# Optimization experiments

Hardware: AMD Instinct MI355X
Metric: run time of the kernel (lower is better)

The kernel has to match this reference:

```python
import jax, jax.numpy as jnp
import numpy as np

TOPK = 13
ALPHA = 1.0
BETA = 6.0
EPS = 1e-9


def _make_boxes(key, shape, img=640.0, min_sz=10.0, max_sz=110.0):
    k1, k2 = jax.random.split(key)
    cxcy = jax.random.uniform(k1, shape[:-1] + (2,)) * img
    wh = min_sz + jax.random.uniform(k2, shape[:-1] + (2,)) * (max_sz - min_sz)
    return jnp.concatenate([cxcy - wh / 2, cxcy + wh / 2], axis=-1)


def setup_inputs() -> dict:
    key = jax.random.key(0)
    ks = jax.random.split(key, 8)
    B, L, C, n, K = 16, 8400, 1, 32, 68
    pred_scores = jax.random.uniform(ks[0], (B, L, C))
    pred_bboxes = _make_boxes(ks[1], (B, L, 4))
    anchor_points = jax.random.uniform(ks[2], (L, 2)) * 640.0
    gt_labels = jax.random.randint(ks[3], (B, n, 1), 0, C).astype(jnp.int64)
    gt_bboxes = _make_boxes(ks[4], (B, n, 4))
    gt_poses = jax.random.normal(ks[5], (B, n, K, 3))
    gt_vertices = jax.random.normal(ks[6], (B, n, K, 3))
    gt_rotations = jax.random.normal(ks[7], (B, n, 3, 3))
    pad_gt_mask = jnp.ones((B, n, 1), jnp.float32)
    return {"pred_scores": pred_scores, "pred_bboxes": pred_bboxes,
            "anchor_points": anchor_points, "gt_labels": gt_labels,
            "gt_bboxes": gt_bboxes, "gt_poses": gt_poses,
            "gt_vertices": gt_vertices, "gt_rotations": gt_rotations,
            "pad_gt_mask": pad_gt_mask, "bg_index": 1}


def batch_iou_similarity(box1, box2):
    # box1 [B,n,4], box2 [B,L,4] -> [B,n,L]
    b1 = box1[:, :, None, :]
    b2 = box2[:, None, :, :]
    x1y1 = jnp.maximum(b1[..., :2], b2[..., :2])
    x2y2 = jnp.minimum(b1[..., 2:], b2[..., 2:])
    overlap = jnp.clip(x2y2 - x1y1, 0).prod(-1)
    area1 = jnp.clip(b1[..., 2:] - b1[..., :2], 0).prod(-1)
    area2 = jnp.clip(b2[..., 2:] - b2[..., :2], 0).prod(-1)
    return overlap / (area1 + area2 - overlap + EPS)


def check_points_inside_bboxes(points, bboxes):
    # points [L,2], bboxes [B,n,4] -> [B,n,L] float
    x = points[None, None, :, 0]
    y = points[None, None, :, 1]
    xmin, ymin, xmax, ymax = jnp.split(bboxes[:, :, None, :], 4, axis=-1)
    deltas = jnp.stack([x - xmin[..., 0], y - ymin[..., 0],
                        xmax[..., 0] - x, ymax[..., 0] - y], axis=-1)
    return (deltas.min(-1) > EPS).astype(bboxes.dtype)


def gather_topk_anchors(metrics, topk, topk_mask):
    # metrics [B,n,L], topk_mask [B,n,1] -> [B,n,L]
    L = metrics.shape[-1]
    _, topk_idxs = jax.lax.top_k(metrics, topk)  # [B,n,topk]
    is_in_topk = jax.nn.one_hot(topk_idxs, L, dtype=metrics.dtype).sum(-2)
    return is_in_topk * topk_mask


def compute_max_iou_anchor(ious):
    # [B,n,L] -> one-hot over gt dim of per-anchor argmax iou
    n = ious.shape[1]
    idx = ious.argmax(axis=1)  # [B,L]
    return jnp.transpose(jax.nn.one_hot(idx, n, dtype=ious.dtype), (0, 2, 1))


def reference(pred_scores, pred_bboxes, anchor_points, gt_labels, gt_bboxes,
              gt_poses, gt_vertices, gt_rotations, pad_gt_mask, bg_index):
    B, L, C = pred_scores.shape
    n = gt_bboxes.shape[1]
    K = gt_poses.shape[2]

    ious = batch_iou_similarity(gt_bboxes, pred_bboxes)  # [B,n,L]
    ps_t = jnp.transpose(pred_scores, (0, 2, 1))  # [B,C,L]
    lbl = gt_labels[..., 0]  # [B,n]
    bbox_cls_scores = jnp.take_along_axis(ps_t, lbl[:, :, None], axis=1)  # [B,n,L]

    alignment_metrics = (bbox_cls_scores ** ALPHA) * (ious ** BETA)
    is_in_gts = check_points_inside_bboxes(anchor_points, gt_bboxes)
    is_in_topk = gather_topk_anchors(alignment_metrics * is_in_gts, TOPK, pad_gt_mask)
    mask_positive = is_in_topk * is_in_gts * pad_gt_mask  # [B,n,L]
    mask_positive_sum = mask_positive.sum(axis=1)  # [B,L]

    # resolve anchors assigned to multiple gts by max IoU (no-op when none)
    mask_multiple = jnp.broadcast_to((mask_positive_sum[:, None, :] > 1), mask_positive.shape)
    is_max_iou = compute_max_iou_anchor(ious)
    mask_positive = jnp.where(mask_multiple, is_max_iou, mask_positive)
    mask_positive_sum = mask_positive.sum(axis=1)

    batch_ind = jnp.arange(B, dtype=jnp.int32)[:, None]
    assigned_gt_index = mask_positive.argmax(axis=1)  # [B,L]
    assigned_gt_index = assigned_gt_index + batch_ind * n
    flat_idx = assigned_gt_index.reshape(-1)

    assigned_labels = gt_labels.reshape(-1)[flat_idx].reshape(B, L)
    assigned_labels = jnp.where(mask_positive_sum > 0, assigned_labels, bg_index)

    assigned_bboxes = gt_bboxes.reshape(-1, 4)[flat_idx].reshape(B, L, 4)
    assigned_poses = gt_poses.reshape(-1, K, 3)[flat_idx].reshape(B, L, K, 3)
    assigned_vertices = gt_vertices.reshape(-1, K, 3)[flat_idx].reshape(B, L, K, 3)
    assigned_rotations = gt_rotations.reshape(-1, 3, 3)[flat_idx].reshape(B, L, 3, 3)

    scores_oh = jax.nn.one_hot(assigned_labels, C + 1, dtype=pred_scores.dtype)
    keep = jnp.array([i for i in range(C + 1) if i != bg_index], dtype=jnp.int32)
    assigned_scores = scores_oh[..., keep]  # [B,L,C]

    am = alignment_metrics * mask_positive
    max_metrics_per_instance = am.max(axis=-1, keepdims=True)
    max_ious_per_instance = (ious * mask_positive).max(axis=-1, keepdims=True)
    am = am / (max_metrics_per_instance + EPS) * max_ious_per_instance
    am = am.max(axis=1)[:, :, None]  # [B,L,1]
    assigned_scores = assigned_scores * am

    return (assigned_labels, assigned_bboxes, assigned_scores, assigned_poses,
            assigned_vertices, assigned_rotations, assigned_gt_index)
```

## Files before the change

### kernel.cpp

```cpp
#include <hip/hip_runtime.h>

#define Bn 16
#define Ln 8400
#define Cn 1
#define Ngt 32
#define Kpt 68
#define TOPKN 13
#define EPSF 1e-9f
#define CAP 2048

typedef unsigned int u32;
typedef float f4v __attribute__((ext_vector_type(4)));

#define OFF_LABELS   0
#define OFF_BBOXES   134400
#define OFF_SCORES   672000
#define OFF_POSES    806400
#define OFF_VERTS    28224000
#define OFF_ROT      55641600
#define OFF_GTIDX    56851200

__device__ __forceinline__ float iou_box(float gx0, float gy0, float gx1, float gy1,
                                         float4 p) {
    float ix0 = fmaxf(gx0, p.x), iy0 = fmaxf(gy0, p.y);
    float ix1 = fminf(gx1, p.z), iy1 = fminf(gy1, p.w);
    float ov = fmaxf(ix1 - ix0, 0.f) * fmaxf(iy1 - iy0, 0.f);
    float a1 = fmaxf(gx1 - gx0, 0.f) * fmaxf(gy1 - gy0, 0.f);
    float a2 = fmaxf(p.z - p.x, 0.f) * fmaxf(p.w - p.y, 0.f);
    return ov / (a1 + a2 - ov + EPSF);
}

__global__ void __launch_bounds__(256) k1_topk(
    const float* __restrict__ pred_scores, const float* __restrict__ pred_bboxes,
    const float* __restrict__ anchors, const int* __restrict__ gt_labels,
    const float* __restrict__ gt_bboxes, const float* __restrict__ pad_mask,
    u32* __restrict__ posmask)
{
    __shared__ float cmet[CAP];
    __shared__ int   cidx[CAP];
    __shared__ int   count;
    __shared__ float rv[4];
    __shared__ int   rl[4], rc[4];
    __shared__ int   sel[TOPKN];

    const int bi = blockIdx.x;
    const int b = bi >> 5, i = bi & 31;
    const int tid = threadIdx.x;

    if (pad_mask[bi] == 0.f) return;

    const float gx0 = gt_bboxes[bi*4+0];
    const float gy0 = gt_bboxes[bi*4+1];
    const float gx1 = gt_bboxes[bi*4+2];
    const float gy1 = gt_bboxes[bi*4+3];
    const int   label = gt_labels[bi];

    const float4* pb = (const float4*)(pred_bboxes + (size_t)b * Ln * 4);
    const float*  ps = pred_scores + (size_t)b * Ln * Cn;
    const float2* ap = (const float2*)anchors;

    if (tid == 0) count = 0;
    __syncthreads();

    for (int l = tid; l < Ln; l += 256) {
        float2 av = ap[l];
        float dmin = fminf(fminf(av.x - gx0, av.y - gy0),
                           fminf(gx1 - av.x, gy1 - av.y));
        if (dmin > EPSF) {
            float4 pv = pb[l];
            float iou = iou_box(gx0, gy0, gx1, gy1, pv);
            float sc = ps[l * Cn + label];
            float i2 = iou * iou;
            float m = sc * (i2 * i2 * i2);
            if (m > 0.f) {
                int c = atomicAdd(&count, 1);
                if (c < CAP) { cmet[c] = m; cidx[c] = l; }
            }
        }
    }
    __syncthreads();
    int p = min(count, CAP);

    if (p > TOPKN) {
        for (int t = 0; t < TOPKN; t++) {
            float bv = -1.f; int bl = 1 << 30, bc = 0;
            for (int c = tid; c < p; c += 256) {
                float v = cmet[c];
                int l = cidx[c];
                if (v > bv || (v == bv && l < bl)) { bv = v; bl = l; bc = c; }
            }
            #pragma unroll
            for (int off = 32; off > 0; off >>= 1) {
                float ov = __shfl_down(bv, off);
                int ol = __shfl_down(bl, off);
                int oc = __shfl_down(bc, off);
                if (ov > bv || (ov == bv && ol < bl)) { bv = ov; bl = ol; bc = oc; }
            }
            int w = tid >> 6;
            if ((tid & 63) == 0) { rv[w] = bv; rl[w] = bl; rc[w] = bc; }
            __syncthreads();
            if (tid == 0) {
                float fv = rv[0]; int fl = rl[0], fc = rc[0];
                #pragma unroll
                for (int w2 = 1; w2 < 4; w2++) {
                    if (rv[w2] > fv || (rv[w2] == fv && rl[w2] < fl)) {
                        fv = rv[w2]; fl = rl[w2]; fc = rc[w2];
                    }
                }
                sel[t] = fl;
                cmet[fc] = -1.f;
            }
            __syncthreads();
        }
        if (tid < TOPKN) atomicOr(&posmask[(size_t)b * Ln + sel[tid]], 1u << i);
    } else {
        if (tid < p) atomicOr(&posmask[(size_t)b * Ln + cidx[tid]], 1u << i);
        if (tid == 0) {
            int need = TOPKN - p;
            for (int l = 0; need > 0 && l < Ln; l++) {
                bool isc = false;
                for (int j = 0; j < p; j++) isc |= (cidx[j] == l);
                if (isc) continue;
                need--;
                float2 av = ap[l];
                float dmin = fminf(fminf(av.x - gx0, av.y - gy0),
                                   fminf(gx1 - av.x, gy1 - av.y));
                if (dmin > EPSF) atomicOr(&posmask[(size_t)b * Ln + l], 1u << i);
            }
        }
    }
}

__global__ void __launch_bounds__(256) k2_resolve(
    const float* __restrict__ pred_scores, const float* __restrict__ pred_bboxes,
    const int* __restrict__ gt_labels, const float* __restrict__ gt_bboxes,
    const u32* __restrict__ posmask, u32* __restrict__ finalmask,
    int* __restrict__ srcidx, float* __restrict__ met_sel,
    float* __restrict__ maxm, float* __restrict__ maxiou)
{
    int bl = blockIdx.x * 256 + threadIdx.x;
    if (bl >= Bn * Ln) return;
    int b = bl / Ln;
    u32 pm = posmask[bl];
    u32 fm = pm;
    float4 pbox = ((const float4*)pred_bboxes)[bl];
    const float4* gb = (const float4*)(gt_bboxes + (size_t)b * Ngt * 4);
    if (__popc(pm) > 1) {
        float best = -1.f; int bi2 = 0;
        for (int i = 0; i < Ngt; i++) {
            float4 g = gb[i];
            float v = iou_box(g.x, g.y, g.z, g.w, pbox);
            if (v > best) { best = v; bi2 = i; }
        }
        fm = 1u << bi2;
    }
    finalmask[bl] = fm;
    int idx = fm ? (__ffs((int)fm) - 1) : 0;
    int src = b * Ngt + idx;
    srcidx[bl] = src;
    float met = 0.f;
    if (fm) {
        float4 g = gb[idx];
        float iou = iou_box(g.x, g.y, g.z, g.w, pbox);
        float sc = pred_scores[(size_t)bl * Cn + gt_labels[src]];
        float i2 = iou * iou;
        met = sc * (i2 * i2 * i2);
        atomicMax((int*)&maxm[src],   __float_as_int(met));
        atomicMax((int*)&maxiou[src], __float_as_int(iou));
    }
    met_sel[bl] = met;
}

__global__ void __launch_bounds__(256) k3_out(
    const float* __restrict__ gt_poses, const float* __restrict__ gt_verts,
    const u32* __restrict__ finalmask, const int* __restrict__ srcidx,
    const float* __restrict__ met_sel, const float* __restrict__ maxm_a,
    const float* __restrict__ maxiou_a, const int* __restrict__ gt_labels,
    const float* __restrict__ gt_bboxes, const float* __restrict__ gt_rot,
    const int* __restrict__ bg_index_p, float* __restrict__ out)
{
    const int QPER = (Kpt * 3) / 4;
    const int total = Bn * Ln * QPER;
    const int nq = 2 * total;
    const int nrot = Bn * Ln * 9;
    int t = blockIdx.x * 256 + threadIdx.x;
    if (t < nq) {
        const float* ga = gt_poses;
        f4v* outp = (f4v*)(out + OFF_POSES);
        int qq = t;
        if (qq >= total) { qq -= total; ga = gt_verts; outp = (f4v*)(out + OFF_VERTS); }
        int bl = qq / QPER;
        int r = qq - bl * QPER;
        int src = srcidx[bl];
        f4v v = ((const f4v*)ga)[src * QPER + r];
        __builtin_nontemporal_store(v, &outp[qq]);
        return;
    }
    t -= nq;
    if (t < nrot) {
        int bl = t / 9;
        int j = t - bl * 9;
        int src = srcidx[bl];
        __builtin_nontemporal_store(gt_rot[src * 9 + j], &out[OFF_ROT + t]);
        return;
    }
    int bl = t - nrot;
    if (bl >= Bn * Ln) return;
    const int bg = *bg_index_p;
    u32 fm = finalmask[bl];
    int src = srcidx[bl];
    int label = fm ? gt_labels[src] : bg;
    float am = 0.f;
    if (fm) am = met_sel[bl] / (maxm_a[src] + EPSF) * maxiou_a[src];
    int keep0 = (bg == 0) ? 1 : 0;
    float sc = (label == keep0) ? am : 0.f;

    __builtin_nontemporal_store((float)label, &out[OFF_LABELS + bl]);
    __builtin_nontemporal_store(sc,           &out[OFF_SCORES + bl]);
    __builtin_nontemporal_store((float)src,   &out[OFF_GTIDX  + bl]);
    f4v bb = ((const f4v*)gt_bboxes)[src];
    __builtin_nontemporal_store(bb, &((f4v*)(out + OFF_BBOXES))[bl]);
}

extern "C" void kernel_launch(void* const* d_in, const int* in_sizes, int n_in,
                              void* d_out, int out_size, void* d_ws, size_t ws_size,
                              hipStream_t stream)
{
    const float* pred_scores = (const float*)d_in[0];
    const float* pred_bboxes = (const float*)d_in[1];
    const float* anchors     = (const float*)d_in[2];
    const int*   gt_labels   = (const int*)d_in[3];
    const float* gt_bboxes   = (const float*)d_in[4];
    const float* gt_poses    = (const float*)d_in[5];
    const float* gt_verts    = (const float*)d_in[6];
    const float* gt_rot      = (const float*)d_in[7];
    const float* pad_mask    = (const float*)d_in[8];
    const int*   bg_index    = (const int*)d_in[9];

    const int nBL = Bn * Ln;
    u32*   posmask  = (u32*)d_ws;
    float* maxm     = (float*)(posmask + nBL);
    float* maxiou   = maxm + Bn * Ngt;
    u32*   finalmask= (u32*)(maxiou + Bn * Ngt);
    int*   srcidx   = (int*)(finalmask + nBL);
    float* met_sel  = (float*)(srcidx + nBL);

    (void)hipMemsetAsync(posmask, 0, ((size_t)nBL + 2 * Bn * Ngt) * sizeof(u32), stream);

    k1_topk<<<Bn * Ngt, 256, 0, stream>>>(pred_scores, pred_bboxes, anchors,
                                          gt_labels, gt_bboxes, pad_mask, posmask);
    k2_resolve<<<(nBL + 255) / 256, 256, 0, stream>>>(pred_scores, pred_bboxes,
                                                      gt_labels, gt_bboxes, posmask,
                                                      finalmask, srcidx, met_sel,
                                                      maxm, maxiou);
    const int nq = 2 * Bn * Ln * ((Kpt * 3) / 4);
    const int nrot = Bn * Ln * 9;
    const int ntot = nq + nrot + nBL;
    k3_out<<<(ntot + 255) / 256, 256, 0, stream>>>(gt_poses, gt_verts, finalmask,
                                                   srcidx, met_sel, maxm, maxiou,
                                                   gt_labels, gt_bboxes, gt_rot,
                                                   bg_index, (float*)d_out);
}
```

Measured before the change: 308.5 us.

## Replace posmask atomics and memset with per-GT top-k index lists, fuse pose/vertex copies

k1 now writes each GT's 13 selected anchor indices to a compact list instead of atomically OR-ing bits into a B×L mask. It also zeroes the max buffers itself, which removes the memset of the full mask. k2 rebuilds the positive mask per anchor by scanning the shared-memory index lists for its batch. k3 makes each thread copy both the pose and the vertex float4 for one slot, halving the thread count for that section. The cost is 416 comparisons per anchor in k2. Zeroing maxm inside k1 depends on kernel ordering before k2's atomicMax, which holds on a single stream.

```diff
diff --git a/kernel.cpp b/kernel.cpp
--- a/kernel.cpp
+++ b/kernel.cpp
@@ -34,7 +34,7 @@
     const float* __restrict__ pred_scores, const float* __restrict__ pred_bboxes,
     const float* __restrict__ anchors, const int* __restrict__ gt_labels,
     const float* __restrict__ gt_bboxes, const float* __restrict__ pad_mask,
-    u32* __restrict__ posmask)
+    int* __restrict__ selg, float* __restrict__ maxm )
 {
     __shared__ float cmet[CAP];
     __shared__ int   cidx[CAP];
@@ -44,10 +44,15 @@
     __shared__ int   sel[TOPKN];
 
     const int bi = blockIdx.x;
-    const int b = bi >> 5, i = bi & 31;
+    const int b = bi >> 5;
     const int tid = threadIdx.x;
 
-    if (pad_mask[bi] == 0.f) return;
+    { int z = bi * 256 + tid; if (z < 2 * Bn * Ngt) maxm[z] = 0.f; }
+
+    if (pad_mask[bi] == 0.f) {
+        if (tid < TOPKN) selg[bi * TOPKN + tid] = -1;
+        return;
+    }
 
     const float gx0 = gt_bboxes[bi*4+0];
     const float gy0 = gt_bboxes[bi*4+1];
@@ -112,20 +117,20 @@
             }
             __syncthreads();
         }
-        if (tid < TOPKN) atomicOr(&posmask[(size_t)b * Ln + sel[tid]], 1u << i);
+        if (tid < TOPKN) selg[bi * TOPKN + tid] = sel[tid];
     } else {
-        if (tid < p) atomicOr(&posmask[(size_t)b * Ln + cidx[tid]], 1u << i);
+        if (tid < p) selg[bi * TOPKN + tid] = cidx[tid];
         if (tid == 0) {
-            int need = TOPKN - p;
-            for (int l = 0; need > 0 && l < Ln; l++) {
+            int pos = p;
+            for (int l = 0; pos < TOPKN && l < Ln; l++) {
                 bool isc = false;
                 for (int j = 0; j < p; j++) isc |= (cidx[j] == l);
                 if (isc) continue;
-                need--;
                 float2 av = ap[l];
                 float dmin = fminf(fminf(av.x - gx0, av.y - gy0),
                                    fminf(gx1 - av.x, gy1 - av.y));
-                if (dmin > EPSF) atomicOr(&posmask[(size_t)b * Ln + l], 1u << i);
+                selg[bi * TOPKN + pos] = (dmin > EPSF) ? l : -1;
+                pos++;
             }
         }
     }
@@ -134,14 +139,28 @@
 __global__ void __launch_bounds__(256) k2_resolve(
     const float* __restrict__ pred_scores, const float* __restrict__ pred_bboxes,
     const int* __restrict__ gt_labels, const float* __restrict__ gt_bboxes,
-    const u32* __restrict__ posmask, u32* __restrict__ finalmask,
+    const int* __restrict__ selg, u32* __restrict__ finalmask,
     int* __restrict__ srcidx, float* __restrict__ met_sel,
     float* __restrict__ maxm, float* __restrict__ maxiou)
 {
-    int bl = blockIdx.x * 256 + threadIdx.x;
-    if (bl >= Bn * Ln) return;
-    int b = bl / Ln;
-    u32 pm = posmask[bl];
+    __shared__ int ssel[Ngt * TOPKN];
+    const int b = blockIdx.y;
+    const int l = blockIdx.x * 256 + threadIdx.x;
+    for (int z = threadIdx.x; z < Ngt * TOPKN; z += 256)
+        ssel[z] = selg[b * Ngt * TOPKN + z];
+    __syncthreads();
+    if (l >= Ln) return;
+    const int bl = b * Ln + l;
+
+    u32 pm = 0;
+    #pragma unroll 4
+    for (int i = 0; i < Ngt; i++) {
+        u32 hit = 0;
+        #pragma unroll
+        for (int j = 0; j < TOPKN; j++) hit |= (u32)(ssel[i * TOPKN + j] == l);
+        pm |= hit << i;
+    }
+
     u32 fm = pm;
     float4 pbox = ((const float4*)pred_bboxes)[bl];
     const float4* gb = (const float4*)(gt_bboxes + (size_t)b * Ngt * 4);
@@ -180,23 +199,20 @@
     const int* __restrict__ bg_index_p, float* __restrict__ out)
 {
     const int QPER = (Kpt * 3) / 4;
-    const int total = Bn * Ln * QPER;
-    const int nq = 2 * total;
+    const int totalA = Bn * Ln * QPER;
     const int nrot = Bn * Ln * 9;
     int t = blockIdx.x * 256 + threadIdx.x;
-    if (t < nq) {
-        const float* ga = gt_poses;
-        f4v* outp = (f4v*)(out + OFF_POSES);
-        int qq = t;
-        if (qq >= total) { qq -= total; ga = gt_verts; outp = (f4v*)(out + OFF_VERTS); }
-        int bl = qq / QPER;
-        int r = qq - bl * QPER;
+    if (t < totalA) {
+        int bl = t / QPER;
+        int r = t - bl * QPER;
         int src = srcidx[bl];
-        f4v v = ((const f4v*)ga)[src * QPER + r];
-        __builtin_nontemporal_store(v, &outp[qq]);
+        f4v pv = ((const f4v*)gt_poses)[src * QPER + r];
+        f4v vv = ((const f4v*)gt_verts)[src * QPER + r];
+        __builtin_nontemporal_store(pv, &((f4v*)(out + OFF_POSES))[t]);
+        __builtin_nontemporal_store(vv, &((f4v*)(out + OFF_VERTS))[t]);
         return;
     }
-    t -= nq;
+    t -= totalA;
     if (t < nrot) {
         int bl = t / 9;
         int j = t - bl * 9;
@@ -238,24 +254,23 @@
     const int*   bg_index    = (const int*)d_in[9];
 
     const int nBL = Bn * Ln;
-    u32*   posmask  = (u32*)d_ws;
-    float* maxm     = (float*)(posmask + nBL);
+    int*   selg     = (int*)d_ws;
+    float* maxm     = (float*)(selg + Bn * Ngt * TOPKN);
     float* maxiou   = maxm + Bn * Ngt;
     u32*   finalmask= (u32*)(maxiou + Bn * Ngt);
     int*   srcidx   = (int*)(finalmask + nBL);
     float* met_sel  = (float*)(srcidx + nBL);
 
-    (void)hipMemsetAsync(posmask, 0, ((size_t)nBL + 2 * Bn * Ngt) * sizeof(u32), stream);
 
     k1_topk<<<Bn * Ngt, 256, 0, stream>>>(pred_scores, pred_bboxes, anchors,
-                                          gt_labels, gt_bboxes, pad_mask, posmask);
-    k2_resolve<<<(nBL + 255) / 256, 256, 0, stream>>>(pred_scores, pred_bboxes,
-                                                      gt_labels, gt_bboxes, posmask,
-                                                      finalmask, srcidx, met_sel,
-                                                      maxm, maxiou);
-    const int nq = 2 * Bn * Ln * ((Kpt * 3) / 4);
+                                          gt_labels, gt_bboxes, pad_mask,
+                                          selg, maxm);
+    k2_resolve<<<dim3((Ln + 255) / 256, Bn), 256, 0, stream>>>(
+        pred_scores, pred_bboxes, gt_labels, gt_bboxes, selg,
+        finalmask, srcidx, met_sel, maxm, maxiou);
+    const int totalA = Bn * Ln * ((Kpt * 3) / 4);
     const int nrot = Bn * Ln * 9;
-    const int ntot = nq + nrot + nBL;
+    const int ntot = totalA + nrot + nBL;
     k3_out<<<(ntot + 255) / 256, 256, 0, stream>>>(gt_poses, gt_verts, finalmask,
                                                    srcidx, met_sel, maxm, maxiou,
                                                    gt_labels, gt_bboxes, gt_rot,
```

Result: faster. 299.8 us (-2.8%).
